# Optimization experiments

Hardware: AMD Instinct MI355X
Metric: run time of the kernel (lower is better)

The kernel has to match this reference:

```python
import jax, jax.numpy as jnp
import numpy as np

N_NODES = 50000
N_EDGES = 800000
IN_CH, HID_CH, OUT_CH = 128, 128, 64


def setup_inputs() -> dict:
    key = jax.random.key(0)
    ks = jax.random.split(key, 8)
    x = jax.random.normal(ks[0], (N_NODES, IN_CH), dtype=jnp.float32)
    edge_index = jax.random.randint(ks[1], (2, N_EDGES), 0, N_NODES, dtype=jnp.int64)
    # PyG SAGEConv params: lin_l (applied to aggregated neighbors, has bias),
    # lin_r (applied to root node, no bias). Stored here as [in, out] matrices.
    s1 = 1.0 / np.sqrt(IN_CH)
    s2 = 1.0 / np.sqrt(HID_CH)
    W1l = jax.random.uniform(ks[2], (IN_CH, HID_CH), jnp.float32, -s1, s1)
    b1 = jnp.zeros((HID_CH,), jnp.float32)
    W1r = jax.random.uniform(ks[3], (IN_CH, HID_CH), jnp.float32, -s1, s1)
    W2l = jax.random.uniform(ks[4], (HID_CH, OUT_CH), jnp.float32, -s2, s2)
    b2 = jnp.zeros((OUT_CH,), jnp.float32)
    W2r = jax.random.uniform(ks[5], (HID_CH, OUT_CH), jnp.float32, -s2, s2)
    return {"x": x, "edge_index": edge_index, "W1l": W1l, "b1": b1,
            "W1r": W1r, "W2l": W2l, "b2": b2, "W2r": W2r}


def _sage_conv(x, src, dst, Wl, b, Wr):
    # mean-aggregate source features onto targets, then linear transform
    msg = x[src]                                        # [E, d] gather
    agg = jax.ops.segment_sum(msg, dst, num_segments=N_NODES)   # [N, d]
    deg = jax.ops.segment_sum(jnp.ones((src.shape[0],), x.dtype), dst,
                              num_segments=N_NODES)     # [N]
    mean = agg / jnp.maximum(deg, 1.0)[:, None]
    return mean @ Wl + b + x @ Wr


def reference(x, edge_index, W1l, b1, W1r, W2l, b2, W2r):
    src, dst = edge_index[0], edge_index[1]
    h = jax.nn.relu(_sage_conv(x, src, dst, W1l, b1, W1r))
    # F.dropout(p=0.3) is identity in eval mode
    return _sage_conv(h, src, dst, W2l, b2, W2r)
```

## Files before the change

### kernel.cpp

```cpp
#include <hip/hip_runtime.h>
#include <hip/hip_bf16.h>


#define TBLOCK 256
#define MAXBUCK 1024

typedef __attribute__((ext_vector_type(8))) short short8;
typedef __attribute__((ext_vector_type(4))) float f32x4;

__device__ __forceinline__ float bf2f(ushort u) {
    union { unsigned int i; float f; } v;
    v.i = (unsigned int)u << 16;
    return v.f;
}
__device__ __forceinline__ ushort f2bf(float f) {
    union { float f; unsigned int u; } v;
    v.f = f;
    unsigned int r = v.u + 0x7fffu + ((v.u >> 16) & 1u);
    return (ushort)(r >> 16);
}

__global__ void detect_k(const int* __restrict__ edges, int* __restrict__ flag) {
    int tid = threadIdx.x;
    int bad = 0;
    for (int i = tid; i < 2048; i += TBLOCK)
        if (edges[2 * i + 1] != 0) bad = 1;
    unsigned long long b = __ballot(bad);
    __shared__ int sbad[4];
    int w = tid >> 6;
    if ((tid & 63) == 0) sbad[w] = (b != 0) ? 1 : 0;
    __syncthreads();
    if (tid == 0) flag[0] = (sbad[0] | sbad[1] | sbad[2] | sbad[3]) ? 0 : 1;
}

__device__ __forceinline__ int load_src(const int* e, long long i, int E, int is64) {
    return is64 ? e[2 * i] : e[i];
}
__device__ __forceinline__ int load_dst(const int* e, long long i, int E, int is64) {
    return is64 ? e[2 * (long long)E + 2 * i] : e[(long long)E + i];
}

__global__ __launch_bounds__(TBLOCK) void histA_k(const int* __restrict__ edges, int E,
                                                  const int* __restrict__ flag,
                                                  int* __restrict__ hist, int NBUCK) {
    __shared__ int lh[MAXBUCK];
    int t = threadIdx.x;
    for (int i = t; i < NBUCK; i += TBLOCK) lh[i] = 0;
    __syncthreads();
    int is64 = flag[0];
    int per = (E + gridDim.x - 1) / gridDim.x;
    int b0 = blockIdx.x * per, b1 = min(E, b0 + per);
    for (int i = b0 + t; i < b1; i += TBLOCK) {
        int d = load_dst(edges, i, E, is64);
        atomicAdd(&lh[d >> 8], 1);
    }
    __syncthreads();
    for (int i = t; i < NBUCK; i += TBLOCK)
        if (lh[i]) atomicAdd(&hist[i], lh[i]);
}

__global__ __launch_bounds__(TBLOCK) void scanB_k(const int* __restrict__ hist,
                                                  int* __restrict__ base,
                                                  int* __restrict__ cursor, int NBUCK) {
    __shared__ int s[TBLOCK];
    int t = threadIdx.x;
    int v[4];
    int sum = 0;
#pragma unroll
    for (int i = 0; i < 4; i++) {
        int idx = t * 4 + i;
        int d = (idx < NBUCK) ? hist[idx] : 0;
        v[i] = sum;
        sum += d;
    }
    s[t] = sum;
    __syncthreads();
    for (int off = 1; off < TBLOCK; off <<= 1) {
        int x = (t >= off) ? s[t - off] : 0;
        __syncthreads();
        s[t] += x;
        __syncthreads();
    }
    int excl = (t == 0) ? 0 : s[t - 1];
#pragma unroll
    for (int i = 0; i < 4; i++) {
        int idx = t * 4 + i;
        if (idx < NBUCK) {
            int b = excl + v[i];
            base[idx] = b;
            cursor[idx] = b;
        }
    }
    if (t == TBLOCK - 1) base[NBUCK] = s[TBLOCK - 1];
}

__global__ __launch_bounds__(TBLOCK) void scatterA_k(const int* __restrict__ edges, int E,
                                                     const int* __restrict__ flag,
                                                     int* __restrict__ cursor,
                                                     unsigned int* __restrict__ packed,
                                                     int NBUCK) {
    __shared__ int lh[MAXBUCK];
    __shared__ int lb[MAXBUCK];
    int t = threadIdx.x;
    for (int i = t; i < NBUCK; i += TBLOCK) lh[i] = 0;
    __syncthreads();
    int is64 = flag[0];
    int per = (E + gridDim.x - 1) / gridDim.x;
    int b0 = blockIdx.x * per, b1 = min(E, b0 + per);
    for (int i = b0 + t; i < b1; i += TBLOCK) {
        int d = load_dst(edges, i, E, is64);
        atomicAdd(&lh[d >> 8], 1);
    }
    __syncthreads();
    for (int i = t; i < NBUCK; i += TBLOCK) {
        int c = lh[i];
        lb[i] = c ? atomicAdd(&cursor[i], c) : 0;
        lh[i] = 0;
    }
    __syncthreads();
    for (int i = b0 + t; i < b1; i += TBLOCK) {
        int s = load_src(edges, i, E, is64);
        int d = load_dst(edges, i, E, is64);
        int b = d >> 8;
        int pos = lb[b] + atomicAdd(&lh[b], 1);
        packed[pos] = (unsigned int)s | ((unsigned int)(d & 255) << 24);
    }
}

__global__ __launch_bounds__(TBLOCK) void buildB_k(const unsigned int* __restrict__ packed,
                                                   const int* __restrict__ base,
                                                   int* __restrict__ offs,
                                                   int* __restrict__ degi,
                                                   float* __restrict__ invdeg,
                                                   int* __restrict__ csr, int N) {
    __shared__ int cnt[TBLOCK], scn[TBLOCK], cur[TBLOCK];
    int t = threadIdx.x;
    int bucket = blockIdx.x;
    int e0 = base[bucket], e1 = base[bucket + 1];
    cnt[t] = 0;
    cur[t] = 0;
    __syncthreads();
    for (int i = e0 + t; i < e1; i += TBLOCK)
        atomicAdd(&cnt[packed[i] >> 24], 1);
    __syncthreads();
    scn[t] = cnt[t];
    __syncthreads();
    for (int off = 1; off < TBLOCK; off <<= 1) {
        int x = (t >= off) ? scn[t - off] : 0;
        __syncthreads();
        scn[t] += x;
        __syncthreads();
    }
    int excl = (t == 0) ? 0 : scn[t - 1];
    int node = bucket * 256 + t;
    if (node < N) {
        offs[node] = e0 + excl;
        degi[node] = cnt[t];
        invdeg[node] = 1.0f / fmaxf((float)cnt[t], 1.0f);
    }
    __syncthreads();
    cnt[t] = excl;
    __syncthreads();
    for (int i = e0 + t; i < e1; i += TBLOCK) {
        unsigned int p = packed[i];
        int nl = p >> 24;
        int pos = e0 + cnt[nl] + atomicAdd(&cur[nl], 1);
        csr[pos] = (int)(p & 0xFFFFFFu);
    }
}

__global__ __launch_bounds__(TBLOCK) void cvtx_k(const float* __restrict__ x,
                                                 ushort* __restrict__ xb, int n8) {
    int i = blockIdx.x * TBLOCK + threadIdx.x;
    if (i >= n8) return;
    const float4* p = (const float4*)x + (size_t)i * 2;
    float4 a = p[0], b = p[1];
    short8 o;
    o[0] = f2bf(a.x); o[1] = f2bf(a.y); o[2] = f2bf(a.z); o[3] = f2bf(a.w);
    o[4] = f2bf(b.x); o[5] = f2bf(b.y); o[6] = f2bf(b.z); o[7] = f2bf(b.w);
    *(short8*)(xb + (size_t)i * 8) = o;
}

__global__ __launch_bounds__(TBLOCK) void cvtw_k(const float* __restrict__ W1l,
                                                 const float* __restrict__ W1r,
                                                 const float* __restrict__ W2l,
                                                 const float* __restrict__ W2r,
                                                 ushort* __restrict__ wc1,
                                                 ushort* __restrict__ wc2) {
    int i = blockIdx.x * TBLOCK + threadIdx.x;
    if (i < 32768) {
        int j = i & 7;
        int rest = i >> 3;
        int n = rest & 127;
        int k = ((rest >> 7) << 3) | j;
        float w = (k < 128) ? W1l[k * 128 + n] : W1r[(k - 128) * 128 + n];
        wc1[i] = f2bf(w);
    } else if (i < 49152) {
        int i2 = i - 32768;
        int j = i2 & 7;
        int rest = i2 >> 3;
        int n = rest & 127;
        int k = ((rest >> 7) << 3) | j;
        float w = (n < 64) ? W2l[k * 64 + n] : W2r[k * 64 + (n - 64)];
        wc2[i2] = f2bf(w);
    }
}

template <int C, bool ACCUM>
__global__ __launch_bounds__(TBLOCK) void gatherb_k(const ushort* __restrict__ feat,
                                                    const int* __restrict__ csr,
                                                    const int* __restrict__ offs,
                                                    const int* __restrict__ degi,
                                                    const float* __restrict__ invdeg,
                                                    ushort* __restrict__ outB,
                                                    float* __restrict__ outF, int N) {
    constexpr int G = C / 8;
    constexpr int NPB = TBLOCK / G;
    int n = blockIdx.x * NPB + threadIdx.x / G;
    if (n >= N) return;
    int lane = threadIdx.x % G;
    int c = lane * 8;
    int s0 = offs[n];
    int d = degi[n];
    float acc[8] = {0.f, 0.f, 0.f, 0.f, 0.f, 0.f, 0.f, 0.f};
    for (int base = 0; base < d; base += G) {
        int rem = d - base;
        int my = (lane < rem) ? csr[s0 + base + lane] : 0;
        if (rem >= G) {
#pragma unroll
            for (int j = 0; j < G; j++) {
                int s = __shfl(my, j, G);
                short8 v = *(const short8*)(feat + (size_t)s * C + c);
#pragma unroll
                for (int q = 0; q < 8; q++) acc[q] += bf2f((ushort)v[q]);
            }
        } else {
            for (int j = 0; j < rem; j++) {
                int s = __shfl(my, j, G);
                short8 v = *(const short8*)(feat + (size_t)s * C + c);
#pragma unroll
                for (int q = 0; q < 8; q++) acc[q] += bf2f((ushort)v[q]);
            }
        }
    }
    float sc = invdeg[n];
    if (ACCUM) {
        float* o = outF + (size_t)n * C + c;
        float4 p0 = *(float4*)o;
        float4 p1 = *(float4*)(o + 4);
        p0.x += sc * acc[0]; p0.y += sc * acc[1]; p0.z += sc * acc[2]; p0.w += sc * acc[3];
        p1.x += sc * acc[4]; p1.y += sc * acc[5]; p1.z += sc * acc[6]; p1.w += sc * acc[7];
        *(float4*)o = p0;
        *(float4*)(o + 4) = p1;
    } else {
        short8 o;
#pragma unroll
        for (int q = 0; q < 8; q++) o[q] = f2bf(sc * acc[q]);
        *(short8*)(outB + (size_t)n * C + c) = o;
    }
}

template <int KTOT, int EPI>
__global__ __launch_bounds__(TBLOCK) void gemm_k(const ushort* __restrict__ A0,
                                                 const ushort* __restrict__ A1,
                                                 const ushort* __restrict__ wc,
                                                 const float* __restrict__ bias,
                                                 ushort* __restrict__ outB,
                                                 float* __restrict__ outF, int N) {
    __shared__ __align__(16) ushort sW[KTOT * 128];
    for (int i = threadIdx.x * 8; i < KTOT * 128; i += TBLOCK * 8)
        *(short8*)&sW[i] = *(const short8*)&wc[i];
    __syncthreads();

    const int wave = threadIdx.x >> 6;
    const int lane = threadIdx.x & 63;
    const int quad = lane >> 4;
    const int l16 = lane & 15;
    const int m0 = (blockIdx.x * 4 + wave) * 32;
    if (m0 >= N) return;

    f32x4 acc[2][8];
#pragma unroll
    for (int t = 0; t < 2; t++)
#pragma unroll
        for (int nt = 0; nt < 8; nt++) acc[t][nt] = (f32x4){0.f, 0.f, 0.f, 0.f};

    const int k0q = quad * 8;
#pragma unroll
    for (int kb = 0; kb < KTOT; kb += 32) {
        int k = kb + k0q;
        const ushort* abase = (KTOT == 256 && k >= 128) ? (A1 + (k - 128)) : (A0 + k);
        short8 a[2];
#pragma unroll
        for (int t = 0; t < 2; t++) {
            int m = m0 + t * 16 + l16;
            if (m > N - 1) m = N - 1;
            a[t] = *(const short8*)(abase + (size_t)m * 128);
        }
#pragma unroll
        for (int nt = 0; nt < 8; nt++) {
            short8 b = *(const short8*)&sW[((k >> 3) * 128 + nt * 16 + l16) * 8];
            acc[0][nt] = __builtin_amdgcn_mfma_f32_16x16x32_bf16(a[0], b, acc[0][nt], 0, 0, 0);
            acc[1][nt] = __builtin_amdgcn_mfma_f32_16x16x32_bf16(a[1], b, acc[1][nt], 0, 0, 0);
        }
    }

#pragma unroll
    for (int t = 0; t < 2; t++) {
#pragma unroll
        for (int r = 0; r < 4; r++) {
            int m = m0 + t * 16 + quad * 4 + r;
            if (m >= N) continue;
#pragma unroll
            for (int nt = 0; nt < 8; nt++) {
                int n = nt * 16 + l16;
                float v = acc[t][nt][r];
                if (EPI == 1) {
                    v = fmaxf(v + bias[n], 0.f);
                    outB[(size_t)m * 128 + n] = f2bf(v);
                } else {
                    if (n < 64) outB[(size_t)m * 64 + n] = f2bf(v);
                    else outF[(size_t)m * 64 + (n - 64)] = v + bias[n - 64];
                }
            }
        }
    }
}

extern "C" void kernel_launch(void* const* d_in, const int* in_sizes, int n_in,
                              void* d_out, int out_size, void* d_ws, size_t ws_size,
                              hipStream_t stream) {
    const float* x = (const float*)d_in[0];
    const int* edges = (const int*)d_in[1];
    const float* W1l = (const float*)d_in[2];
    const float* b1 = (const float*)d_in[3];
    const float* W1r = (const float*)d_in[4];
    const float* W2l = (const float*)d_in[5];
    const float* b2 = (const float*)d_in[6];
    const float* W2r = (const float*)d_in[7];
    float* out = (float*)d_out;

    const int N = in_sizes[0] / 128;
    const int E = in_sizes[1] / 2;
    const int Na = (N + 63) & ~63;
    const int NBUCK = (N + 255) >> 8;

    char* W = (char*)d_ws;
    size_t off = 0;
    auto alloc = [&](size_t bytes) {
        void* p = W + off;
        off = (off + bytes + 255) & ~(size_t)255;
        return p;
    };
    int* flag = (int*)alloc(4);
    int* hist = (int*)alloc((size_t)MAXBUCK * 4);
    size_t zbytes = off;
    int* base = (int*)alloc((size_t)(MAXBUCK + 1) * 4);
    int* cursor = (int*)alloc((size_t)MAXBUCK * 4);
    int* offs = (int*)alloc((size_t)Na * 4);
    int* degi = (int*)alloc((size_t)Na * 4);
    float* invdeg = (float*)alloc((size_t)Na * 4);
    unsigned int* packed = (unsigned int*)alloc((size_t)E * 4);
    int* csr = (int*)alloc((size_t)E * 4);
    ushort* xb = (ushort*)alloc((size_t)N * 128 * 2);
    ushort* agg1b = (ushort*)alloc((size_t)N * 128 * 2);
    ushort* hb = (ushort*)alloc((size_t)N * 128 * 2);
    ushort* t2b = (ushort*)alloc((size_t)N * 64 * 2);
    ushort* wc1 = (ushort*)alloc(32768 * 2);
    ushort* wc2 = (ushort*)alloc(16384 * 2);

    hipMemsetAsync(d_ws, 0, zbytes, stream);

    detect_k<<<1, TBLOCK, 0, stream>>>(edges, flag);
    histA_k<<<64, TBLOCK, 0, stream>>>(edges, E, flag, hist, NBUCK);
    scanB_k<<<1, TBLOCK, 0, stream>>>(hist, base, cursor, NBUCK);
    scatterA_k<<<64, TBLOCK, 0, stream>>>(edges, E, flag, cursor, packed, NBUCK);
    buildB_k<<<NBUCK, TBLOCK, 0, stream>>>(packed, base, offs, degi, invdeg, csr, N);

    cvtx_k<<<(N * 128 / 8 + TBLOCK - 1) / TBLOCK, TBLOCK, 0, stream>>>(x, xb, N * 128 / 8);
    cvtw_k<<<192, TBLOCK, 0, stream>>>(W1l, W1r, W2l, W2r, wc1, wc2);

    gatherb_k<128, false><<<(N + 15) / 16, TBLOCK, 0, stream>>>(
        xb, csr, offs, degi, invdeg, agg1b, nullptr, N);
    gemm_k<256, 1><<<(N + 127) / 128, TBLOCK, 0, stream>>>(
        agg1b, xb, wc1, b1, hb, nullptr, N);

    gemm_k<128, 2><<<(N + 127) / 128, TBLOCK, 0, stream>>>(
        hb, nullptr, wc2, b2, t2b, out, N);
    gatherb_k<64, true><<<(N + 31) / 32, TBLOCK, 0, stream>>>(
        t2b, csr, offs, degi, invdeg, nullptr, out, N);
}
```

Baseline: 229.3 us.

## Inline dtype detection, widen CSR build grids, merge conversion kernels

Removes the standalone detect kernel by having every histogram and scatter block redundantly detect whether the edge indices are int64. The histogram and scatter grids grow from 64 to 512 blocks so the edge passes use more of the GPU. The x and weight conversion kernels are merged into one launch. Together these cut two kernel launches and their serialization gaps, at the cost of each block doing an extra 2048-element probe read and more global atomics on the bucket histogram and cursors.

```diff
diff --git a/kernel.cpp b/kernel.cpp
--- a/kernel.cpp
+++ b/kernel.cpp
@@ -4,6 +4,7 @@
 
 #define TBLOCK 256
 #define MAXBUCK 1024
+#define BUILD_GRID 512
 
 typedef __attribute__((ext_vector_type(8))) short short8;
 typedef __attribute__((ext_vector_type(4))) float f32x4;
@@ -20,17 +21,19 @@
     return (ushort)(r >> 16);
 }
 
-__global__ void detect_k(const int* __restrict__ edges, int* __restrict__ flag) {
+__device__ __forceinline__ int block_detect_is64(const int* __restrict__ edges) {
+    __shared__ int sbad[4];
+    __shared__ int sflag;
     int tid = threadIdx.x;
     int bad = 0;
     for (int i = tid; i < 2048; i += TBLOCK)
         if (edges[2 * i + 1] != 0) bad = 1;
     unsigned long long b = __ballot(bad);
-    __shared__ int sbad[4];
-    int w = tid >> 6;
-    if ((tid & 63) == 0) sbad[w] = (b != 0) ? 1 : 0;
-    __syncthreads();
-    if (tid == 0) flag[0] = (sbad[0] | sbad[1] | sbad[2] | sbad[3]) ? 0 : 1;
+    if ((tid & 63) == 0) sbad[tid >> 6] = (b != 0) ? 1 : 0;
+    __syncthreads();
+    if (tid == 0) sflag = (sbad[0] | sbad[1] | sbad[2] | sbad[3]) ? 0 : 1;
+    __syncthreads();
+    return sflag;
 }
 
 __device__ __forceinline__ int load_src(const int* e, long long i, int E, int is64) {
@@ -41,13 +44,12 @@
 }
 
 __global__ __launch_bounds__(TBLOCK) void histA_k(const int* __restrict__ edges, int E,
-                                                  const int* __restrict__ flag,
                                                   int* __restrict__ hist, int NBUCK) {
+    int is64 = block_detect_is64(edges);
     __shared__ int lh[MAXBUCK];
     int t = threadIdx.x;
     for (int i = t; i < NBUCK; i += TBLOCK) lh[i] = 0;
     __syncthreads();
-    int is64 = flag[0];
     int per = (E + gridDim.x - 1) / gridDim.x;
     int b0 = blockIdx.x * per, b1 = min(E, b0 + per);
     for (int i = b0 + t; i < b1; i += TBLOCK) {
@@ -95,16 +97,15 @@
 }
 
 __global__ __launch_bounds__(TBLOCK) void scatterA_k(const int* __restrict__ edges, int E,
-                                                     const int* __restrict__ flag,
                                                      int* __restrict__ cursor,
                                                      unsigned int* __restrict__ packed,
                                                      int NBUCK) {
+    int is64 = block_detect_is64(edges);
     __shared__ int lh[MAXBUCK];
     __shared__ int lb[MAXBUCK];
     int t = threadIdx.x;
     for (int i = t; i < NBUCK; i += TBLOCK) lh[i] = 0;
     __syncthreads();
-    int is64 = flag[0];
     int per = (E + gridDim.x - 1) / gridDim.x;
     int b0 = blockIdx.x * per, b1 = min(E, b0 + per);
     for (int i = b0 + t; i < b1; i += TBLOCK) {
@@ -169,40 +170,42 @@
     }
 }
 
-__global__ __launch_bounds__(TBLOCK) void cvtx_k(const float* __restrict__ x,
-                                                 ushort* __restrict__ xb, int n8) {
-    int i = blockIdx.x * TBLOCK + threadIdx.x;
-    if (i >= n8) return;
-    const float4* p = (const float4*)x + (size_t)i * 2;
-    float4 a = p[0], b = p[1];
-    short8 o;
-    o[0] = f2bf(a.x); o[1] = f2bf(a.y); o[2] = f2bf(a.z); o[3] = f2bf(a.w);
-    o[4] = f2bf(b.x); o[5] = f2bf(b.y); o[6] = f2bf(b.z); o[7] = f2bf(b.w);
-    *(short8*)(xb + (size_t)i * 8) = o;
-}
-
-__global__ __launch_bounds__(TBLOCK) void cvtw_k(const float* __restrict__ W1l,
+__global__ __launch_bounds__(TBLOCK) void prep_k(const float* __restrict__ x,
+                                                 const float* __restrict__ W1l,
                                                  const float* __restrict__ W1r,
                                                  const float* __restrict__ W2l,
                                                  const float* __restrict__ W2r,
+                                                 ushort* __restrict__ xb,
                                                  ushort* __restrict__ wc1,
-                                                 ushort* __restrict__ wc2) {
-    int i = blockIdx.x * TBLOCK + threadIdx.x;
-    if (i < 32768) {
-        int j = i & 7;
-        int rest = i >> 3;
-        int n = rest & 127;
-        int k = ((rest >> 7) << 3) | j;
-        float w = (k < 128) ? W1l[k * 128 + n] : W1r[(k - 128) * 128 + n];
-        wc1[i] = f2bf(w);
-    } else if (i < 49152) {
-        int i2 = i - 32768;
-        int j = i2 & 7;
-        int rest = i2 >> 3;
-        int n = rest & 127;
-        int k = ((rest >> 7) << 3) | j;
-        float w = (n < 64) ? W2l[k * 64 + n] : W2r[k * 64 + (n - 64)];
-        wc2[i2] = f2bf(w);
+                                                 ushort* __restrict__ wc2,
+                                                 int n8, int nxb) {
+    if ((int)blockIdx.x < nxb) {
+        int i = blockIdx.x * TBLOCK + threadIdx.x;
+        if (i >= n8) return;
+        const float4* p = (const float4*)x + (size_t)i * 2;
+        float4 a = p[0], b = p[1];
+        short8 o;
+        o[0] = f2bf(a.x); o[1] = f2bf(a.y); o[2] = f2bf(a.z); o[3] = f2bf(a.w);
+        o[4] = f2bf(b.x); o[5] = f2bf(b.y); o[6] = f2bf(b.z); o[7] = f2bf(b.w);
+        *(short8*)(xb + (size_t)i * 8) = o;
+    } else {
+        int i = (blockIdx.x - nxb) * TBLOCK + threadIdx.x;
+        if (i < 32768) {
+            int j = i & 7;
+            int rest = i >> 3;
+            int n = rest & 127;
+            int k = ((rest >> 7) << 3) | j;
+            float w = (k < 128) ? W1l[k * 128 + n] : W1r[(k - 128) * 128 + n];
+            wc1[i] = f2bf(w);
+        } else if (i < 49152) {
+            int i2 = i - 32768;
+            int j = i2 & 7;
+            int rest = i2 >> 3;
+            int n = rest & 127;
+            int k = ((rest >> 7) << 3) | j;
+            float w = (n < 64) ? W2l[k * 64 + n] : W2r[k * 64 + (n - 64)];
+            wc2[i2] = f2bf(w);
+        }
     }
 }
 
@@ -352,7 +355,6 @@
         off = (off + bytes + 255) & ~(size_t)255;
         return p;
     };
-    int* flag = (int*)alloc(4);
     int* hist = (int*)alloc((size_t)MAXBUCK * 4);
     size_t zbytes = off;
     int* base = (int*)alloc((size_t)(MAXBUCK + 1) * 4);
@@ -371,14 +373,14 @@
 
     hipMemsetAsync(d_ws, 0, zbytes, stream);
 
-    detect_k<<<1, TBLOCK, 0, stream>>>(edges, flag);
-    histA_k<<<64, TBLOCK, 0, stream>>>(edges, E, flag, hist, NBUCK);
+    histA_k<<<BUILD_GRID, TBLOCK, 0, stream>>>(edges, E, hist, NBUCK);
     scanB_k<<<1, TBLOCK, 0, stream>>>(hist, base, cursor, NBUCK);
-    scatterA_k<<<64, TBLOCK, 0, stream>>>(edges, E, flag, cursor, packed, NBUCK);
+    scatterA_k<<<BUILD_GRID, TBLOCK, 0, stream>>>(edges, E, cursor, packed, NBUCK);
     buildB_k<<<NBUCK, TBLOCK, 0, stream>>>(packed, base, offs, degi, invdeg, csr, N);
 
-    cvtx_k<<<(N * 128 / 8 + TBLOCK - 1) / TBLOCK, TBLOCK, 0, stream>>>(x, xb, N * 128 / 8);
-    cvtw_k<<<192, TBLOCK, 0, stream>>>(W1l, W1r, W2l, W2r, wc1, wc2);
+    const int n8 = N * 128 / 8;
+    const int nxb = (n8 + TBLOCK - 1) / TBLOCK;
+    prep_k<<<nxb + 192, TBLOCK, 0, stream>>>(x, W1l, W1r, W2l, W2r, xb, wc1, wc2, n8, nxb);
 
     gatherb_k<128, false><<<(N + 15) / 16, TBLOCK, 0, stream>>>(
         xb, csr, offs, degi, invdeg, agg1b, nullptr, N);
```

New measurement: 215.9 us. -5.9%, faster.
